# Optimization experiments

Measured on AMD Instinct MI355X. Metric: run time of the kernel, lower is better.

The kernel has to match this reference:

```python
import jax, jax.numpy as jnp
import numpy as np

N_NODES = 100000
N_EDGES = 3200000
NFEAT, NHID, NCLASS = 512, 256, 40


def setup_inputs() -> dict:
    key = jax.random.key(0)
    ks = jax.random.split(key, 8)
    x = jax.random.normal(ks[0], (N_NODES, NFEAT), dtype=jnp.float32)
    edge_src = jax.random.randint(ks[1], (N_EDGES,), 0, N_NODES, dtype=jnp.int32)
    edge_dst = jax.random.randint(ks[2], (N_EDGES,), 0, N_NODES, dtype=jnp.int32)
    # normalized adjacency values (e.g. D^-1/2 A D^-1/2 entries)
    edge_weight = jax.random.uniform(ks[3], (N_EDGES,), dtype=jnp.float32)
    W1 = jax.random.normal(ks[4], (NFEAT, NHID), dtype=jnp.float32) * (1.0 / np.sqrt(NFEAT))
    b1 = jnp.zeros((NHID,), dtype=jnp.float32)
    W2 = jax.random.normal(ks[5], (NHID, NCLASS), dtype=jnp.float32) * (1.0 / np.sqrt(NHID))
    b2 = jnp.zeros((NCLASS,), dtype=jnp.float32)
    return {"x": x, "edge_src": edge_src, "edge_dst": edge_dst,
            "edge_weight": edge_weight, "W1": W1, "b1": b1, "W2": W2, "b2": b2}


def _gcn_conv(x, edge_src, edge_dst, edge_weight, W, b):
    # GCNConv: support = x @ W ; out = spmm(adj, support) + b
    support = x @ W                                   # [N, D_out]
    msgs = edge_weight[:, None] * support[edge_src]   # [E, D_out]
    agg = jax.ops.segment_sum(msgs, edge_dst, num_segments=x.shape[0])
    return agg + b


def reference(x, edge_src, edge_dst, edge_weight, W1, b1, W2, b2):
    h = jax.nn.relu(_gcn_conv(x, edge_src, edge_dst, edge_weight, W1, b1))
    # F.dropout with training=False is identity (eval/reference mode)
    h = _gcn_conv(h, edge_src, edge_dst, edge_weight, W2, b2)
    return jax.nn.log_softmax(h, axis=1)
```

## Files before the change

kernel.cpp:

```cpp
#include <hip/hip_runtime.h>
#include <hip/hip_bf16.h>
#include <math.h>


#define NFEAT 512
#define NHID  256
#define NCLASS 40

typedef __attribute__((ext_vector_type(4))) float f32x4;
typedef __attribute__((ext_vector_type(8))) short s16x8;

__device__ __forceinline__ ushort f2bf(float f) {
  unsigned u = __float_as_uint(f);
  u = (u + 0x7fffu + ((u >> 16) & 1u)) >> 16;
  return (ushort)u;
}
__device__ __forceinline__ float bflo(unsigned u) {
  return __uint_as_float(u << 16);
}
__device__ __forceinline__ float bfhi(unsigned u) {
  return __uint_as_float(u & 0xffff0000u);
}

__global__ __launch_bounds__(256) void w1t_kernel(const float* __restrict__ W1,
                                                  ushort* __restrict__ Bt) {
  int idx = blockIdx.x * 256 + threadIdx.x;
  int k = idx >> 8, n = idx & 255;
  Bt[n * NFEAT + k] = f2bf(W1[idx]);
}

#define LDK 40
__global__ __launch_bounds__(256) void gemm1_mfma(
    const float* __restrict__ A, const ushort* __restrict__ Bt,
    ushort* __restrict__ C, int M) {
  __shared__ ushort As[128 * LDK];
  __shared__ ushort Bs[128 * LDK];
  int tid = threadIdx.x;
  int wave = tid >> 6, lane = tid & 63;
  int bm = blockIdx.y * 128;
  int bn = blockIdx.x * 128;
  int wm = (wave & 1) * 64, wn = (wave >> 1) * 64;
  int lm = lane & 15;
  int lk = (lane >> 4) * 8;

  int arow = tid >> 1;
  int ahalf = (tid & 1) * 16;
  int brow = tid >> 2;
  int bq = (tid & 3) * 8;

  f32x4 acc[4][4] = {};

  const bool arv = (bm + arow) < M;
  const float* aptr = A + (size_t)(bm + arow) * NFEAT + ahalf;
  ushort* asp = &As[arow * LDK + ahalf];

  for (int k0 = 0; k0 < NFEAT; k0 += 32) {
#pragma unroll
    for (int q = 0; q < 4; ++q) {
      float4 v = arv ? *(const float4*)(aptr + k0 + q * 4)
                     : make_float4(0.f, 0.f, 0.f, 0.f);
      ushort4 b;
      b.x = f2bf(v.x); b.y = f2bf(v.y); b.z = f2bf(v.z); b.w = f2bf(v.w);
      *(ushort4*)(asp + q * 4) = b;
    }
#pragma unroll
    for (int p = 0; p < 2; ++p) {
      int n = p * 64 + brow;
      *(uint4*)&Bs[n * LDK + bq] =
          *(const uint4*)&Bt[(size_t)(bn + n) * NFEAT + k0 + bq];
    }
    __syncthreads();
    s16x8 afr[4], bfr[4];
#pragma unroll
    for (int i = 0; i < 4; ++i)
      afr[i] = *(const s16x8*)&As[(wm + i * 16 + lm) * LDK + lk];
#pragma unroll
    for (int j = 0; j < 4; ++j)
      bfr[j] = *(const s16x8*)&Bs[(wn + j * 16 + lm) * LDK + lk];
#pragma unroll
    for (int i = 0; i < 4; ++i)
#pragma unroll
      for (int j = 0; j < 4; ++j)
        acc[i][j] = __builtin_amdgcn_mfma_f32_16x16x32_bf16(afr[i], bfr[j],
                                                            acc[i][j], 0, 0, 0);
    __syncthreads();
  }
  int ocol = bn + wn + lm;
  int orow0 = bm + wm + (lane >> 4) * 4;
#pragma unroll
  for (int i = 0; i < 4; ++i) {
#pragma unroll
    for (int r = 0; r < 4; ++r) {
      int row = orow0 + i * 16 + r;
      if (row < M) {
#pragma unroll
        for (int j = 0; j < 4; ++j)
          C[(size_t)row * NHID + ocol + j * 16] = f2bf(acc[i][j][r]);
      }
    }
  }
}

__global__ __launch_bounds__(256) void hist_kernel(const int* __restrict__ dst,
                                                   int* __restrict__ deg, int E) {
  int e = blockIdx.x * 256 + threadIdx.x;
  if (e < E) atomicAdd(&deg[dst[e]], 1);
}

__global__ __launch_bounds__(256) void scan1_kernel(const int* __restrict__ deg,
                                                    int* __restrict__ part,
                                                    int* __restrict__ bsums, int M) {
  __shared__ int tmp[256];
  int t = threadIdx.x;
  int i = blockIdx.x * 256 + t;
  int v = (i < M) ? deg[i] : 0;
  tmp[t] = v;
  __syncthreads();
  for (int off = 1; off < 256; off <<= 1) {
    int add = (t >= off) ? tmp[t - off] : 0;
    __syncthreads();
    tmp[t] += add;
    __syncthreads();
  }
  if (i < M) part[i] = tmp[t];
  if (t == 255) bsums[blockIdx.x] = tmp[255];
}

__global__ __launch_bounds__(512) void scan2_kernel(int* __restrict__ bsums, int nb) {
  __shared__ int tmp[512];
  int t = threadIdx.x;
  int v = (t < nb) ? bsums[t] : 0;
  tmp[t] = v;
  __syncthreads();
  for (int off = 1; off < 512; off <<= 1) {
    int add = (t >= off) ? tmp[t - off] : 0;
    __syncthreads();
    tmp[t] += add;
    __syncthreads();
  }
  if (t < nb) bsums[t] = tmp[t];
}

__global__ __launch_bounds__(256) void scan3_kernel(
    const int* __restrict__ part, const int* __restrict__ bsums,
    const int* __restrict__ deg, int* __restrict__ rowptr,
    int* __restrict__ cursor, int M) {
  int i = blockIdx.x * 256 + threadIdx.x;
  if (i >= M) return;
  int incl = part[i] + (blockIdx.x > 0 ? bsums[blockIdx.x - 1] : 0);
  int start = incl - deg[i];
  rowptr[i] = start;
  cursor[i] = start;
}

__global__ __launch_bounds__(256) void scatter_kernel(
    const int* __restrict__ src, const int* __restrict__ dst,
    const float* __restrict__ w, int* __restrict__ cursor,
    int2* __restrict__ ep, int E) {
  int e = blockIdx.x * 256 + threadIdx.x;
  if (e >= E) return;
  int d = dst[e];
  int pos = atomicAdd(&cursor[d], 1);
  ep[pos] = make_int2(src[e], __float_as_int(w[e]));
}

__global__ __launch_bounds__(256) void spmm1_csr_kernel(
    const ushort* __restrict__ S, const int* __restrict__ rowptr,
    const int* __restrict__ deg, const int2* __restrict__ ep,
    const float* __restrict__ b1, ushort* __restrict__ h, int M) {
  int wid = (blockIdx.x * 256 + threadIdx.x) >> 6;
  int lane = threadIdx.x & 63;
  if (wid >= M) return;
  int beg = rowptr[wid];
  int n = deg[wid];
  const ushort* Sl = S + (size_t)lane * 4;
  float acc0 = 0.f, acc1 = 0.f, acc2 = 0.f, acc3 = 0.f;
  for (int j0 = 0; j0 < n; j0 += 64) {
    int cnt = min(64, n - j0);
    int msrc = 0;
    float mw = 0.f;
    if (lane < cnt) {
      int2 e = ep[beg + j0 + lane];
      msrc = e.x;
      mw = __int_as_float(e.y);
    }
    for (int j = 0; j < cnt; ++j) {
      int s = __shfl(msrc, j);
      float wt = __shfl(mw, j);
      uint2 u = *(const uint2*)(Sl + ((size_t)s << 8));
      acc0 += wt * bflo(u.x);
      acc1 += wt * bfhi(u.x);
      acc2 += wt * bflo(u.y);
      acc3 += wt * bfhi(u.y);
    }
  }
  float4 b = *(const float4*)(b1 + lane * 4);
  ushort4 o;
  o.x = f2bf(fmaxf(acc0 + b.x, 0.f));
  o.y = f2bf(fmaxf(acc1 + b.y, 0.f));
  o.z = f2bf(fmaxf(acc2 + b.z, 0.f));
  o.w = f2bf(fmaxf(acc3 + b.w, 0.f));
  *(ushort4*)(h + ((size_t)wid << 8) + lane * 4) = o;
}

__global__ __launch_bounds__(256) void gemm2_kernel(
    const ushort* __restrict__ H, const float* __restrict__ W2,
    ushort* __restrict__ S2, int M) {
  __shared__ float W2s[NHID * NCLASS];
  for (int i = threadIdx.x; i < NHID * NCLASS; i += 256) W2s[i] = W2[i];
  __syncthreads();
  int row = blockIdx.x * 256 + threadIdx.x;
  if (row >= M) return;
  const float4* W2v = (const float4*)W2s;
  float4 acc[10];
#pragma unroll
  for (int j = 0; j < 10; ++j) acc[j] = make_float4(0.f, 0.f, 0.f, 0.f);
  const uint4* hp = (const uint4*)(H + (size_t)row * NHID);
  for (int kb = 0; kb < 32; ++kb) {
    uint4 u = hp[kb];
    float a[8] = {bflo(u.x), bfhi(u.x), bflo(u.y), bfhi(u.y),
                  bflo(u.z), bfhi(u.z), bflo(u.w), bfhi(u.w)};
#pragma unroll
    for (int kk = 0; kk < 8; ++kk) {
#pragma unroll
      for (int j = 0; j < 10; ++j) {
        float4 wv = W2v[(kb * 8 + kk) * 10 + j];
        acc[j].x += a[kk] * wv.x;
        acc[j].y += a[kk] * wv.y;
        acc[j].z += a[kk] * wv.z;
        acc[j].w += a[kk] * wv.w;
      }
    }
  }
  uint2* outp = (uint2*)(S2 + (size_t)row * NCLASS);
#pragma unroll
  for (int j = 0; j < 10; j += 2) {
    uint2 o0, o1;
    o0.x = (unsigned)f2bf(acc[j].x) | ((unsigned)f2bf(acc[j].y) << 16);
    o0.y = (unsigned)f2bf(acc[j].z) | ((unsigned)f2bf(acc[j].w) << 16);
    o1.x = (unsigned)f2bf(acc[j + 1].x) | ((unsigned)f2bf(acc[j + 1].y) << 16);
    o1.y = (unsigned)f2bf(acc[j + 1].z) | ((unsigned)f2bf(acc[j + 1].w) << 16);
    outp[j] = o0;
    outp[j + 1] = o1;
  }
}

__global__ __launch_bounds__(256) void spmm2_csr_kernel(
    const ushort* __restrict__ S2, const int* __restrict__ rowptr,
    const int* __restrict__ deg, const int2* __restrict__ ep,
    const float* __restrict__ b2, float* __restrict__ out, int M) {
  int wid = (blockIdx.x * 256 + threadIdx.x) >> 6;
  int lane = threadIdx.x & 63;
  if (wid >= M) return;
  int beg = rowptr[wid];
  int n = deg[wid];
  float acc0 = 0.f, acc1 = 0.f;
  const ushort* S2l = S2 + lane * 2;
  for (int j0 = 0; j0 < n; j0 += 64) {
    int cnt = min(64, n - j0);
    int msrc = 0;
    float mw = 0.f;
    if (lane < cnt) {
      int2 e = ep[beg + j0 + lane];
      msrc = e.x;
      mw = __int_as_float(e.y);
    }
    for (int j = 0; j < cnt; ++j) {
      int s = __shfl(msrc, j);
      float wt = __shfl(mw, j);
      if (lane < 20) {
        unsigned u = *(const unsigned*)(S2l + (size_t)s * NCLASS);
        acc0 += wt * bflo(u);
        acc1 += wt * bfhi(u);
      }
    }
  }
  float v0 = -INFINITY, v1 = -INFINITY;
  if (lane < 20) {
    float2 b = *(const float2*)(b2 + lane * 2);
    v0 = acc0 + b.x;
    v1 = acc1 + b.y;
  }
  float m = fmaxf(v0, v1);
#pragma unroll
  for (int off = 32; off; off >>= 1) m = fmaxf(m, __shfl_xor(m, off));
  float ex = (lane < 20) ? __expf(v0 - m) + __expf(v1 - m) : 0.f;
  float s = ex;
#pragma unroll
  for (int off = 32; off; off >>= 1) s += __shfl_xor(s, off);
  float lse = m + __logf(s);
  if (lane < 20) {
    float2 o = {v0 - lse, v1 - lse};
    *(float2*)(out + (size_t)wid * NCLASS + lane * 2) = o;
  }
}

extern "C" void kernel_launch(void* const* d_in, const int* in_sizes, int n_in,
                              void* d_out, int out_size, void* d_ws,
                              size_t ws_size, hipStream_t stream) {
  const float* x  = (const float*)d_in[0];
  const int* esrc = (const int*)d_in[1];
  const int* edst = (const int*)d_in[2];
  const float* ew = (const float*)d_in[3];
  const float* W1 = (const float*)d_in[4];
  const float* b1 = (const float*)d_in[5];
  const float* W2 = (const float*)d_in[6];
  const float* b2 = (const float*)d_in[7];
  float* out = (float*)d_out;

  const int M = in_sizes[0] / NFEAT;
  const int E = in_sizes[1];

  char* p = (char*)d_ws;
  ushort* support1 = (ushort*)p;           p += (size_t)M * NHID * 2;
  ushort* h        = (ushort*)p;           p += (size_t)M * NHID * 2;
  ushort* support2 = (ushort*)p;           p += (size_t)M * NCLASS * 2;
  ushort* W1t      = (ushort*)p;           p += (size_t)NFEAT * NHID * 2;
  int*    deg      = (int*)p;              p += (size_t)M * 4;
  int*    part     = (int*)p;              p += (size_t)M * 4;
  int*    rowptr   = (int*)p;              p += (size_t)M * 4;
  int*    cursor   = (int*)p;              p += (size_t)M * 4;
  int*    bsums    = (int*)p;              p += 512 * 4;
  int2*   ep       = (int2*)p;

  const int nbScan = (M + 255) / 256;

  hipMemsetAsync(deg, 0, (size_t)M * sizeof(int), stream);
  hist_kernel<<<(E + 255) / 256, 256, 0, stream>>>(edst, deg, E);
  scan1_kernel<<<nbScan, 256, 0, stream>>>(deg, part, bsums, M);
  scan2_kernel<<<1, 512, 0, stream>>>(bsums, nbScan);
  scan3_kernel<<<nbScan, 256, 0, stream>>>(part, bsums, deg, rowptr, cursor, M);
  scatter_kernel<<<(E + 255) / 256, 256, 0, stream>>>(esrc, edst, ew, cursor,
                                                      ep, E);

  w1t_kernel<<<(NFEAT * NHID) / 256, 256, 0, stream>>>(W1, W1t);
  dim3 g1(NHID / 128, (M + 127) / 128);
  gemm1_mfma<<<g1, 256, 0, stream>>>(x, W1t, support1, M);
  spmm1_csr_kernel<<<(M * 64 + 255) / 256, 256, 0, stream>>>(
      support1, rowptr, deg, ep, b1, h, M);

  gemm2_kernel<<<(M + 255) / 256, 256, 0, stream>>>(h, W2, support2, M);
  spmm2_csr_kernel<<<(M * 64 + 255) / 256, 256, 0, stream>>>(
      support2, rowptr, deg, ep, b2, out, M);
}
```

Measured before the change: 1.213 ms.

## Replace per-edge global atomic CSR scatter with two-pass bucketed binning

Replaces the per-edge global atomicAdd scatter into the CSR edge array with a two-level counting sort. First, edges are binned into 512-node buckets using shared-memory histograms and one global atomic per bucket per block. Second, each bucket is sorted into final CSR positions using shared-memory cursors. The aim is to cut global atomic contention and random scattered writes, at the cost of an extra pass through a temporary edge buffer and more workspace. The design caps the bucket count at 256, so it assumes M <= 131072 nodes.

```diff
diff --git a/kernel.cpp b/kernel.cpp
--- a/kernel.cpp
+++ b/kernel.cpp
@@ -6,6 +6,10 @@
 #define NFEAT 512
 #define NHID  256
 #define NCLASS 40
+#define BKT_SHIFT 9
+#define BKT_NODES 512
+#define MAX_BKT 256
+#define BIN_EPB 4096
 
 typedef __attribute__((ext_vector_type(4))) float f32x4;
 typedef __attribute__((ext_vector_type(8))) short s16x8;
@@ -143,25 +147,72 @@
 
 __global__ __launch_bounds__(256) void scan3_kernel(
     const int* __restrict__ part, const int* __restrict__ bsums,
-    const int* __restrict__ deg, int* __restrict__ rowptr,
-    int* __restrict__ cursor, int M) {
+    const int* __restrict__ deg, int* __restrict__ rowptr, int M) {
   int i = blockIdx.x * 256 + threadIdx.x;
   if (i >= M) return;
   int incl = part[i] + (blockIdx.x > 0 ? bsums[blockIdx.x - 1] : 0);
-  int start = incl - deg[i];
-  rowptr[i] = start;
-  cursor[i] = start;
-}
-
-__global__ __launch_bounds__(256) void scatter_kernel(
-    const int* __restrict__ src, const int* __restrict__ dst,
-    const float* __restrict__ w, int* __restrict__ cursor,
-    int2* __restrict__ ep, int E) {
-  int e = blockIdx.x * 256 + threadIdx.x;
-  if (e >= E) return;
-  int d = dst[e];
-  int pos = atomicAdd(&cursor[d], 1);
-  ep[pos] = make_int2(src[e], __float_as_int(w[e]));
+  rowptr[i] = incl - deg[i];
+}
+
+__global__ __launch_bounds__(256) void initcur_kernel(
+    const int* __restrict__ rowptr, int* __restrict__ gcursor, int nbkt) {
+  int b = threadIdx.x;
+  if (b < nbkt) gcursor[b] = rowptr[b * BKT_NODES];
+}
+
+__global__ __launch_bounds__(256) void binA_kernel(
+    const int* __restrict__ esrc, const int* __restrict__ edst,
+    const float* __restrict__ ew, int* __restrict__ gcursor,
+    int2* __restrict__ tmp_sw, ushort* __restrict__ tmp_d, int E) {
+  __shared__ int hist[MAX_BKT];
+  int t = threadIdx.x;
+  for (int i = t; i < MAX_BKT; i += 256) hist[i] = 0;
+  __syncthreads();
+  int e0 = blockIdx.x * BIN_EPB;
+#pragma unroll
+  for (int k = 0; k < BIN_EPB / 256; ++k) {
+    int e = e0 + k * 256 + t;
+    if (e < E) atomicAdd(&hist[edst[e] >> BKT_SHIFT], 1);
+  }
+  __syncthreads();
+  for (int i = t; i < MAX_BKT; i += 256) {
+    int c = hist[i];
+    hist[i] = c ? atomicAdd(&gcursor[i], c) : 0;
+  }
+  __syncthreads();
+#pragma unroll
+  for (int k = 0; k < BIN_EPB / 256; ++k) {
+    int e = e0 + k * 256 + t;
+    if (e < E) {
+      int d = edst[e];
+      int b = d >> BKT_SHIFT;
+      int pos = atomicAdd(&hist[b], 1);
+      tmp_sw[pos] = make_int2(esrc[e], __float_as_int(ew[e]));
+      tmp_d[pos] = (ushort)(d & (BKT_NODES - 1));
+    }
+  }
+}
+
+__global__ __launch_bounds__(512) void binB_kernel(
+    const int2* __restrict__ tmp_sw, const ushort* __restrict__ tmp_d,
+    const int* __restrict__ rowptr, int2* __restrict__ ep, int M, int E) {
+  __shared__ int cur[BKT_NODES];
+  int b = blockIdx.x;
+  int nbase = b * BKT_NODES;
+  for (int i = threadIdx.x; i < BKT_NODES; i += 512) {
+    int node = nbase + i;
+    cur[i] = (node < M) ? rowptr[node] : 0;
+  }
+  __syncthreads();
+  int start = rowptr[nbase];
+  int nend = nbase + BKT_NODES;
+  int end = (nend < M) ? rowptr[nend] : E;
+  for (int i = start + threadIdx.x; i < end; i += 512) {
+    int2 sw = tmp_sw[i];
+    int dl = tmp_d[i];
+    int pos = atomicAdd(&cur[dl], 1);
+    ep[pos] = sw;
+  }
 }
 
 __global__ __launch_bounds__(256) void spmm1_csr_kernel(
@@ -310,6 +361,7 @@
 
   const int M = in_sizes[0] / NFEAT;
   const int E = in_sizes[1];
+  const int nbkt = (M + BKT_NODES - 1) / BKT_NODES;
 
   char* p = (char*)d_ws;
   ushort* support1 = (ushort*)p;           p += (size_t)M * NHID * 2;
@@ -319,9 +371,11 @@
   int*    deg      = (int*)p;              p += (size_t)M * 4;
   int*    part     = (int*)p;              p += (size_t)M * 4;
   int*    rowptr   = (int*)p;              p += (size_t)M * 4;
-  int*    cursor   = (int*)p;              p += (size_t)M * 4;
+  int*    gcursor  = (int*)p;              p += MAX_BKT * 4;
   int*    bsums    = (int*)p;              p += 512 * 4;
-  int2*   ep       = (int2*)p;
+  int2*   ep       = (int2*)p;             p += (size_t)E * 8;
+  int2*   tmp_sw   = (int2*)p;             p += (size_t)E * 8;
+  ushort* tmp_d    = (ushort*)p;
 
   const int nbScan = (M + 255) / 256;
 
@@ -329,9 +383,11 @@
   hist_kernel<<<(E + 255) / 256, 256, 0, stream>>>(edst, deg, E);
   scan1_kernel<<<nbScan, 256, 0, stream>>>(deg, part, bsums, M);
   scan2_kernel<<<1, 512, 0, stream>>>(bsums, nbScan);
-  scan3_kernel<<<nbScan, 256, 0, stream>>>(part, bsums, deg, rowptr, cursor, M);
-  scatter_kernel<<<(E + 255) / 256, 256, 0, stream>>>(esrc, edst, ew, cursor,
-                                                      ep, E);
+  scan3_kernel<<<nbScan, 256, 0, stream>>>(part, bsums, deg, rowptr, M);
+  initcur_kernel<<<1, 256, 0, stream>>>(rowptr, gcursor, nbkt);
+  binA_kernel<<<(E + BIN_EPB - 1) / BIN_EPB, 256, 0, stream>>>(
+      esrc, edst, ew, gcursor, tmp_sw, tmp_d, E);
+  binB_kernel<<<nbkt, 512, 0, stream>>>(tmp_sw, tmp_d, rowptr, ep, M, E);
 
   w1t_kernel<<<(NFEAT * NHID) / 256, 256, 0, stream>>>(W1, W1t);
   dim3 g1(NHID / 128, (M + 127) / 128);
```

Result: faster. 1.123 ms (-7.4%).
